# Performance work log

Hardware: AMD Instinct MI355X
Metric: run time of the kernel (lower is better)

The kernel has to match this reference:

```python
import jax, jax.numpy as jnp
import numpy as np

B, N, FI, F, NN, ITER = 128, 64, 8, 32, 64, 3
E = N * (N - 1)  # 4032 directed edges (fully connected, no self-loops)


def _p(k, shape):
    return jax.random.normal(k, shape, jnp.float32) / np.float32(np.sqrt(shape[0]))


def setup_inputs() -> dict:
    key = jax.random.key(0)
    ks = jax.random.split(key, 20)
    u_is = np.array([i for i in range(N) for j in range(N) if i != j], np.int32)
    u_js = np.array([j for i in range(N) for j in range(N) if i != j], np.int32)
    return {
        "node0": jax.random.normal(ks[0], (B, N, FI), jnp.float32),
        "edge": jax.random.normal(ks[1], (B, E, 2), jnp.float32),
        "node_mean": jax.random.normal(ks[2], (B, N, 1), jnp.float32),
        "node_vari": jax.random.uniform(ks[3], (B, N, 1), jnp.float32),
        "h": jax.random.normal(ks[4], (B, N, NN), jnp.float32),
        "W1": _p(ks[5], (FI, F)), "b1": jnp.zeros((F,), jnp.float32),
        "W2a": _p(ks[6], (2 * F + 2, NN)), "b2a": jnp.zeros((NN,), jnp.float32),
        "W2b": _p(ks[7], (NN, NN // 2)), "b2b": jnp.zeros((NN // 2,), jnp.float32),
        "W2c": _p(ks[8], (NN // 2, F)), "b2c": jnp.zeros((F,), jnp.float32),
        "Wx": _p(ks[9], (F, 3 * NN)), "Ux": _p(ks[10], (NN, 3 * NN)),
        "bx": jnp.zeros((3 * NN,), jnp.float32), "bh": jnp.zeros((3 * NN,), jnp.float32),
        "W3b": _p(ks[11], (NN, F)), "b3b": jnp.zeros((F,), jnp.float32),
        "W4a": _p(ks[12], (F, NN)), "b4a": jnp.zeros((NN,), jnp.float32),
        "W4b": _p(ks[13], (NN, NN // 2)), "b4b": jnp.zeros((NN // 2,), jnp.float32),
        "W4c": _p(ks[14], (NN // 2, F)), "b4c": jnp.zeros((F,), jnp.float32),
        "u_is": jnp.asarray(u_is), "u_js": jnp.asarray(u_js),
    }


def _forward(node0, edge, h, W1, b1, W2a, b2a, W2b, b2b, W2c, b2c,
             Wx, Ux, bx, bh, W3b, b3b, W4a, b4a, W4b, b4b, W4c, b4c,
             u_is, u_js):
    gelu = jax.nn.gelu
    node = node0 @ W1 + b1  # fc1a: [B,N,F]
    for _ in range(ITER):
        # gather source/target node features per directed edge, concat edge feats
        u_ij = jnp.concatenate([node[:, u_is, :], node[:, u_js, :], edge], -1)  # [B,E,2F+2]
        m = gelu(u_ij @ W2a + b2a)   # [B,E,NN]
        m = gelu(m @ W2b + b2b)      # [B,E,NN//2]
        m = gelu(m @ W2c + b2c)      # [B,E,F]
        # edges are ordered by source node i, so segment-sum == reshape+sum
        m_i = m.reshape(-1, N, N - 1, F).sum(-2)  # [B,N,F]
        # FlexGRU cell with GELU candidate activation (ACT_GELU)
        gx = m_i @ Wx + bx
        gh = h @ Ux + bh
        xr, xz, xn = jnp.split(gx, 3, -1)
        hr, hz, hn = jnp.split(gh, 3, -1)
        r = jax.nn.sigmoid(xr + hr)
        z = jax.nn.sigmoid(xz + hz)
        n = gelu(xn + r * hn)
        h = (1.0 - z) * n + z * h    # [B,N,NN]
        node = h @ W3b + b3b         # fc3b: [B,N,F]
    # readout: fc4a -> fc4b -> fc4c with no intermediate activation (as in source)
    return ((node @ W4a + b4a) @ W4b + b4b) @ W4c + b4c  # [B,N,F]


def reference(node0, edge, node_mean, node_vari, h, W1, b1, W2a, b2a, W2b, b2b,
              W2c, b2c, Wx, Ux, bx, bh, W3b, b3b, W4a, b4a, W4b, b4b, W4c, b4c,
              u_is, u_js):
    # node_mean / node_vari are accepted by the original forward but unused
    return _forward(node0, edge, h, W1, b1, W2a, b2a, W2b, b2b, W2c, b2c,
                    Wx, Ux, bx, bh, W3b, b3b, W4a, b4a, W4b, b4b, W4c, b4c,
                    u_is, u_js)
```

## Files before the change

kernel.cpp:

```cpp
#include <hip/hip_runtime.h>


typedef _Float16 f16;
typedef _Float16 h8 __attribute__((ext_vector_type(8)));
typedef float f4 __attribute__((ext_vector_type(4)));

#define MFMA16(a, b, c) __builtin_amdgcn_mfma_f32_16x16x32_f16(a, b, c, 0, 0, 0)
#define WFENCE()                        \
  do {                                  \
    __builtin_amdgcn_wave_barrier();    \
    __asm__ volatile("" ::: "memory");  \
  } while (0)

#define H_OFF 0
#define Q_OFF 2097152
#define P_OFF 4194304
#define WQ_OFF 6291456
#define O_W45B 0
#define O_W2BTH 768
#define O_W2BTL 4864
#define O_B2B 8960
#define O_W2CTH 9088
#define O_W2CTL 11136
#define O_B2C 13184

#define LI_M2W 0
#define LI_ND 0
#define LI_HN 1024
#define LI_T1 3072
#define LI_T2 5248
#define LI_W2BH 10240
#define LI_W2BL 14848
#define LI_W2CH 19456
#define LI_W2CL 22016
#define LI_MACC 24576
#define LI_H32 25600
#define LI_TOTAL 27648

__device__ __forceinline__ float fast_rcp(float x) {
#if __has_builtin(__builtin_amdgcn_rcpf)
  return __builtin_amdgcn_rcpf(x);
#else
  return 1.0f / x;
#endif
}
__device__ __forceinline__ float gelu_f(float x) {
  float x3 = x * x * x;
  float u = -1.5957691216057308f * fmaf(0.044715f, x3, x);
  return x * fast_rcp(1.f + __expf(u));
}
__device__ __forceinline__ float sigm_f(float x) {
  return fast_rcp(1.f + __expf(-x));
}
__device__ __forceinline__ void splitw(float v, f16& h, f16& l) {
  h = (f16)v;
  l = (f16)(v - (float)h);
}

__global__ __launch_bounds__(256) void k_pre(
    const float* __restrict__ node0, const float* __restrict__ W1,
    const float* __restrict__ b1, const float* __restrict__ W2a,
    const float* __restrict__ b2a, const float* __restrict__ W2b,
    const float* __restrict__ b2b, const float* __restrict__ W2c,
    const float* __restrict__ b2c, float* __restrict__ ws) {
  const int t = threadIdx.x;
  const int blk = blockIdx.x;
  char* wsb = (char*)ws;
  float* Qbuf = (float*)(wsb + Q_OFF);
  float* Pbuf = (float*)(wsb + P_OFF);
  char* W = wsb + WQ_OFF;

  if (blk < 256) {
    __shared__ float sNode[1024];
    const int b = blk >> 1;
    const int n0 = (blk & 1) << 5;
    for (int idx = t; idx < 1024; idx += 256) {
      const int n = idx >> 5, f = idx & 31;
      float acc = b1[f];
#pragma unroll
      for (int k = 0; k < 8; ++k)
        acc = fmaf(node0[((size_t)(b * 64 + n0 + n)) * 8 + k], W1[k * 32 + f], acc);
      sNode[idx] = acc;
    }
    __syncthreads();
    const int u = t & 63;
    const int sel = (t >> 6) & 1;
    const int nb = t >> 7;
    const float binit = sel ? 0.f : b2a[u];
    float acc[16];
#pragma unroll
    for (int o = 0; o < 16; ++o) acc[o] = binit;
    const float* wcol = W2a + (sel ? 2048 : 0) + u;
#pragma unroll 4
    for (int k = 0; k < 32; ++k) {
      const float w = wcol[k * 64];
#pragma unroll
      for (int o = 0; o < 16; ++o)
        acc[o] = fmaf(sNode[(nb + 2 * o) * 32 + k], w, acc[o]);
    }
    float* dst = sel ? Pbuf : Qbuf;
#pragma unroll
    for (int o = 0; o < 16; ++o)
      dst[((size_t)(b * 64 + n0 + nb + 2 * o)) * 64 + u] = acc[o];
  } else {
    float* wb = (float*)(W + O_W45B);
    if (t < 64) {
      wb[t] = W2a[64 * 64 + t];
      wb[64 + t] = W2a[65 * 64 + t];
      wb[128 + t] = b2a[t];
    }
    f16* bth = (f16*)(W + O_W2BTH);
    f16* btl = (f16*)(W + O_W2BTL);
    for (int idx = t; idx < 2048; idx += 256) {
      const int k = idx >> 5, v = idx & 31;
      f16 h_, l_;
      splitw(W2b[k * 32 + v], h_, l_);
      bth[v * 64 + k] = h_;
      btl[v * 64 + k] = l_;
    }
    float* b2bf = (float*)(W + O_B2B);
    if (t < 32) b2bf[t] = b2b[t];
    f16* cth = (f16*)(W + O_W2CTH);
    f16* ctl = (f16*)(W + O_W2CTL);
    for (int idx = t; idx < 1024; idx += 256) {
      const int k = idx >> 5, v = idx & 31;
      f16 h_, l_;
      splitw(W2c[k * 32 + v], h_, l_);
      cth[v * 32 + k] = h_;
      ctl[v * 32 + k] = l_;
    }
    float* b2cf = (float*)(W + O_B2C);
    if (t < 32) b2cf[t] = b2c[t];
  }
}

__global__ __launch_bounds__(256, 4) void k_iter(
    const float* __restrict__ edge, float* __restrict__ ws,
    const float* __restrict__ h_in, const float* __restrict__ Wx,
    const float* __restrict__ Ux, const float* __restrict__ bx,
    const float* __restrict__ bh, const float* __restrict__ W3b,
    const float* __restrict__ b3b, const float* __restrict__ W2a,
    const float* __restrict__ b2a, const float* __restrict__ W4a,
    const float* __restrict__ b4a, const float* __restrict__ W4b,
    const float* __restrict__ b4b, const float* __restrict__ W4c,
    const float* __restrict__ b4c, float* __restrict__ out, const int is_last) {
  __shared__ alignas(16) char sm[LI_TOTAL];
  f16* sW2BH = (f16*)(sm + LI_W2BH);
  f16* sW2BL = (f16*)(sm + LI_W2BL);
  f16* sW2CH = (f16*)(sm + LI_W2CH);
  f16* sW2CL = (f16*)(sm + LI_W2CL);
  float* sMacc = (float*)(sm + LI_MACC);
  float* sH32 = (float*)(sm + LI_H32);

  const int tid = threadIdx.x;
  const int lane = tid & 63;
  const int wave = tid >> 6;
  const int col = lane & 15;
  const int quad = lane >> 4;
  const int b = blockIdx.x >> 3;
  const int i0 = (blockIdx.x & 7) << 3;

  char* wsb = (char*)ws;
  float* h_ws = (float*)(wsb + H_OFF);
  float* Qbuf = (float*)(wsb + Q_OFF);
  float* Pbuf = (float*)(wsb + P_OFF);
  const char* W = wsb + WQ_OFF;
  const float* w45b = (const float*)(W + O_W45B);
  const f16* W2BTHg = (const f16*)(W + O_W2BTH);
  const f16* W2BTLg = (const f16*)(W + O_W2BTL);
  const float* b2b_g = (const float*)(W + O_B2B);
  const f16* W2CTHg = (const f16*)(W + O_W2CTH);
  const f16* W2CTLg = (const f16*)(W + O_W2CTL);
  const float* b2c_g = (const float*)(W + O_B2C);

  for (int idx = tid; idx < 1024; idx += 256) {
    const int v = idx >> 5, k2 = idx & 31;
    ((unsigned int*)sW2BH)[v * 36 + k2] = ((const unsigned int*)W2BTHg)[idx];
    ((unsigned int*)sW2BL)[v * 36 + k2] = ((const unsigned int*)W2BTLg)[idx];
  }
  for (int idx = tid; idx < 512; idx += 256) {
    const int v = idx >> 4, k2 = idx & 15;
    ((unsigned int*)sW2CH)[v * 20 + k2] = ((const unsigned int*)W2CTHg)[idx];
    ((unsigned int*)sW2CL)[v * 20 + k2] = ((const unsigned int*)W2CTLg)[idx];
  }
  if (tid < 128) {
    const int nl = tid >> 4;
    const int k4 = (tid & 15) * 4;
    *(float4*)(sH32 + tid * 4) =
        *(const float4*)(h_in + ((size_t)(b * 64 + i0 + nl)) * 64 + k4);
  }
  __syncthreads();

  const float bb2[2] = {b2b_g[col], b2b_g[16 + col]};
  const float bc2[2] = {b2c_g[col], b2c_g[16 + col]};
  f4 wav[2][2], wbv[2][2];
#pragma unroll
  for (int kh = 0; kh < 2; ++kh) {
#pragma unroll
    for (int p = 0; p < 2; ++p) {
      wav[kh][p] = *(const f4*)(w45b + kh * 32 + quad * 8 + p * 4);
      wbv[kh][p] = *(const f4*)(w45b + 64 + kh * 32 + quad * 8 + p * 4);
    }
  }
  f16* m2h = (f16*)(sm + LI_M2W + wave * 2560);
  f16* m2l = m2h + 640;

#pragma unroll 1
  for (int cc2 = 0; cc2 < 2; ++cc2) {
    const int c = wave + 4 * cc2;
    const int ig = i0 + c;
    f4 qb[2][2];
#pragma unroll
    for (int kh = 0; kh < 2; ++kh)
#pragma unroll
      for (int p = 0; p < 2; ++p)
        qb[kh][p] = *(const f4*)(Qbuf + ((size_t)(b * 64 + ig)) * 64 + kh * 32 +
                                 quad * 8 + p * 4);
    const float* erow = edge + ((size_t)b * 4032 + (size_t)ig * 63) * 2;
    float ev0[4], ev1[4];
#pragma unroll
    for (int mt = 0; mt < 4; ++mt) {
      const int ko = mt * 16 + col;
      if (ko < 63) {
        const float2 e = *(const float2*)(erow + ko * 2);
        ev0[mt] = e.x;
        ev1[mt] = e.y;
      } else {
        ev0[mt] = 0.f;
        ev1[mt] = 0.f;
      }
    }
    float racc[2] = {0.f, 0.f};
#pragma unroll
    for (int mt = 0; mt < 4; ++mt) {
      const int ko = mt * 16 + col;
      int j = ko + ((ko >= ig) ? 1 : 0);
      j = (j > 63) ? 63 : j;
      const float e0 = ev0[mt], e1 = ev1[mt];
      h8 ah[2], al[2];
#pragma unroll
      for (int kh = 0; kh < 2; ++kh) {
        const float* prow =
            Pbuf + ((size_t)(b * 64 + j)) * 64 + kh * 32 + quad * 8;
        const f4 p0 = *(const f4*)prow;
        const f4 p1 = *(const f4*)(prow + 4);
#pragma unroll
        for (int jj = 0; jj < 4; ++jj) {
          float v = qb[kh][0][jj] + p0[jj];
          v = fmaf(e1, wbv[kh][0][jj], fmaf(e0, wav[kh][0][jj], v));
          float g = gelu_f(v) * 0.015625f;
          f16 hi = (f16)g;
          ah[kh][jj] = hi;
          al[kh][jj] = (f16)(g - (float)hi);
          v = qb[kh][1][jj] + p1[jj];
          v = fmaf(e1, wbv[kh][1][jj], fmaf(e0, wav[kh][1][jj], v));
          g = gelu_f(v) * 0.015625f;
          hi = (f16)g;
          ah[kh][4 + jj] = hi;
          al[kh][4 + jj] = (f16)(g - (float)hi);
        }
      }
#pragma unroll
      for (int nt = 0; nt < 2; ++nt) {
        const f16* rbh = sW2BH + (nt * 16 + col) * 72 + quad * 8;
        const f16* rbl = sW2BL + (nt * 16 + col) * 72 + quad * 8;
        const h8 bh0 = *(const h8*)rbh;
        const h8 bh1 = *(const h8*)(rbh + 32);
        const h8 bl0 = *(const h8*)rbl;
        const h8 bl1 = *(const h8*)(rbl + 32);
        f4 cm = {0.f, 0.f, 0.f, 0.f};
        cm = MFMA16(ah[0], bh0, cm);
        cm = MFMA16(ah[1], bh1, cm);
        cm = MFMA16(ah[0], bl0, cm);
        cm = MFMA16(ah[1], bl1, cm);
        cm = MFMA16(al[0], bh0, cm);
        cm = MFMA16(al[1], bh1, cm);
#pragma unroll
        for (int r = 0; r < 4; ++r) {
          const float g = gelu_f(fmaf(64.f, cm[r], bb2[nt])) * 0.015625f;
          const f16 hi = (f16)g;
          const int o = (quad * 4 + r) * 40 + nt * 16 + col;
          m2h[o] = hi;
          m2l[o] = (f16)(g - (float)hi);
        }
      }
      WFENCE();
      const h8 a2h = *(const h8*)(m2h + col * 40 + quad * 8);
      const h8 a2l = *(const h8*)(m2l + col * 40 + quad * 8);
      WFENCE();
#pragma unroll
      for (int nt = 0; nt < 2; ++nt) {
        const h8 bch = *(const h8*)(sW2CH + (nt * 16 + col) * 40 + quad * 8);
        const h8 bcl = *(const h8*)(sW2CL + (nt * 16 + col) * 40 + quad * 8);
        f4 dm = {0.f, 0.f, 0.f, 0.f};
        dm = MFMA16(a2h, bch, dm);
        dm = MFMA16(a2h, bcl, dm);
        dm = MFMA16(a2l, bch, dm);
#pragma unroll
        for (int r = 0; r < 4; ++r) {
          const int slot3 = mt * 16 + quad * 4 + r;
          const float g = gelu_f(fmaf(64.f, dm[r], bc2[nt]));
          racc[nt] += (slot3 != 63) ? g : 0.f;
        }
      }
    }
    racc[0] += __shfl_xor(racc[0], 16);
    racc[0] += __shfl_xor(racc[0], 32);
    racc[1] += __shfl_xor(racc[1], 16);
    racc[1] += __shfl_xor(racc[1], 32);
    if (lane < 32) sMacc[c * 32 + lane] = (lane < 16) ? racc[0] : racc[1];
  }
  __syncthreads();

  float* sHn = (float*)(sm + LI_HN);
  {
    const int u = lane;
    const float bxr = bx[u], bhr = bh[u];
    const float bxz = bx[64 + u], bhz = bh[64 + u];
    const float bxn = bx[128 + u], bhn = bh[128 + u];
#pragma unroll 1
    for (int p = 0; p < 2; ++p) {
      const int n0 = wave + 4 * p;
      float axr = 0.f, axz = 0.f, axn = 0.f;
#pragma unroll 4
      for (int k = 0; k < 32; ++k) {
        const float m0 = sMacc[n0 * 32 + k];
        axr = fmaf(m0, Wx[k * 192 + u], axr);
        axz = fmaf(m0, Wx[k * 192 + 64 + u], axz);
        axn = fmaf(m0, Wx[k * 192 + 128 + u], axn);
      }
      float ahr = 0.f, ahz = 0.f, ahn = 0.f;
#pragma unroll 4
      for (int k = 0; k < 64; ++k) {
        const float h0 = sH32[n0 * 64 + k];
        ahr = fmaf(h0, Ux[k * 192 + u], ahr);
        ahz = fmaf(h0, Ux[k * 192 + 64 + u], ahz);
        ahn = fmaf(h0, Ux[k * 192 + 128 + u], ahn);
      }
      const float r_ = sigm_f(axr + ahr + bxr + bhr);
      const float z_ = sigm_f(axz + ahz + bxz + bhz);
      const float n_ = gelu_f(fmaf(r_, ahn + bhn, axn + bxn));
      const float hold = sH32[n0 * 64 + u];
      const float hnew = (1.f - z_) * n_ + z_ * hold;
      sHn[n0 * 64 + u] = hnew;
      if (!is_last) h_ws[((size_t)(b * 64 + i0 + n0)) * 64 + u] = hnew;
    }
  }
  __syncthreads();

  float* sNd = (float*)(sm + LI_ND);
  {
    const int nn = tid >> 5, f = tid & 31;
    float acc = b3b[f];
#pragma unroll 8
    for (int k = 0; k < 64; ++k)
      acc = fmaf(sHn[nn * 64 + k], W3b[k * 32 + f], acc);
    sNd[nn * 32 + f] = acc;
  }
  __syncthreads();

  if (!is_last) {
    const int u = lane;
    const int sel = (tid >> 6) & 1;
    const int nb = tid >> 7;
    const float binit = sel ? 0.f : b2a[u];
    float acc[4] = {binit, binit, binit, binit};
    const float* wcol = W2a + (sel ? 2048 : 0) + u;
#pragma unroll 4
    for (int k = 0; k < 32; ++k) {
      const float w = wcol[k * 64];
      acc[0] = fmaf(sNd[(nb + 0) * 32 + k], w, acc[0]);
      acc[1] = fmaf(sNd[(nb + 2) * 32 + k], w, acc[1]);
      acc[2] = fmaf(sNd[(nb + 4) * 32 + k], w, acc[2]);
      acc[3] = fmaf(sNd[(nb + 6) * 32 + k], w, acc[3]);
    }
    float* dst = sel ? Pbuf : Qbuf;
#pragma unroll
    for (int o = 0; o < 4; ++o)
      dst[((size_t)(b * 64 + i0 + nb + 2 * o)) * 64 + u] = acc[o];
  } else {
    float* sT1 = (float*)(sm + LI_T1);
    float* sT2 = (float*)(sm + LI_T2);
    {
      const int u = lane;
      float acc0 = b4a[u], acc1 = b4a[u];
#pragma unroll 4
      for (int k = 0; k < 32; ++k) {
        const float w = W4a[k * 64 + u];
        acc0 = fmaf(sNd[wave * 32 + k], w, acc0);
        acc1 = fmaf(sNd[(wave + 4) * 32 + k], w, acc1);
      }
      sT1[wave * 68 + u] = acc0;
      sT1[(wave + 4) * 68 + u] = acc1;
    }
    __syncthreads();
    {
      const int nn = tid >> 5, v = tid & 31;
      float acc = b4b[v];
#pragma unroll 8
      for (int k = 0; k < 64; ++k)
        acc = fmaf(sT1[nn * 68 + k], W4b[k * 32 + v], acc);
      sT2[nn * 36 + v] = acc;
    }
    __syncthreads();
    {
      const int nn = tid >> 5, f = tid & 31;
      float acc = b4c[f];
#pragma unroll 8
      for (int k = 0; k < 32; ++k)
        acc = fmaf(sT2[nn * 36 + k], W4c[k * 32 + f], acc);
      out[((size_t)(b * 64 + i0 + nn)) * 32 + f] = acc;
    }
  }
}

extern "C" void kernel_launch(void* const* d_in, const int* in_sizes, int n_in,
                              void* d_out, int out_size, void* d_ws, size_t ws_size,
                              hipStream_t stream) {
  (void)in_sizes;
  (void)n_in;
  (void)out_size;
  (void)ws_size;
  const float* node0 = (const float*)d_in[0];
  const float* edge = (const float*)d_in[1];
  const float* hin = (const float*)d_in[4];
  const float* W1 = (const float*)d_in[5];
  const float* b1 = (const float*)d_in[6];
  const float* W2a = (const float*)d_in[7];
  const float* b2a = (const float*)d_in[8];
  const float* W2b = (const float*)d_in[9];
  const float* b2b = (const float*)d_in[10];
  const float* W2c = (const float*)d_in[11];
  const float* b2c = (const float*)d_in[12];
  const float* Wx = (const float*)d_in[13];
  const float* Ux = (const float*)d_in[14];
  const float* bx = (const float*)d_in[15];
  const float* bh = (const float*)d_in[16];
  const float* W3b = (const float*)d_in[17];
  const float* b3b = (const float*)d_in[18];
  const float* W4a = (const float*)d_in[19];
  const float* b4a = (const float*)d_in[20];
  const float* W4b = (const float*)d_in[21];
  const float* b4b = (const float*)d_in[22];
  const float* W4c = (const float*)d_in[23];
  const float* b4c = (const float*)d_in[24];

  float* ws = (float*)d_ws;
  char* wsb = (char*)d_ws;
  float* h_ws = (float*)(wsb + H_OFF);
  float* out = (float*)d_out;

  k_pre<<<dim3(257), dim3(256), 0, stream>>>(node0, W1, b1, W2a, b2a, W2b, b2b, W2c,
                                             b2c, ws);
  k_iter<<<dim3(1024), dim3(256), 0, stream>>>(edge, ws, hin, Wx, Ux, bx, bh, W3b,
                                               b3b, W2a, b2a, W4a, b4a, W4b, b4b,
                                               W4c, b4c, nullptr, 0);
  k_iter<<<dim3(1024), dim3(256), 0, stream>>>(edge, ws, h_ws, Wx, Ux, bx, bh, W3b,
                                               b3b, W2a, b2a, W4a, b4a, W4b, b4b,
                                               W4c, b4c, nullptr, 0);
  k_iter<<<dim3(1024), dim3(256), 0, stream>>>(edge, ws, h_ws, Wx, Ux, bx, bh, W3b,
                                               b3b, W2a, b2a, W4a, b4a, W4b, b4b,
                                               W4c, b4c, out, 1);
}
```

Baseline: 281.1 us.

## Keep W2c fragments in registers, shrink LDS, raise occupancy, split k_pre finer

```diff
diff --git a/kernel.cpp b/kernel.cpp
--- a/kernel.cpp
+++ b/kernel.cpp
@@ -31,11 +31,9 @@
 #define LI_T2 5248
 #define LI_W2BH 10240
 #define LI_W2BL 14848
-#define LI_W2CH 19456
-#define LI_W2CL 22016
-#define LI_MACC 24576
-#define LI_H32 25600
-#define LI_TOTAL 27648
+#define LI_MACC 19456
+#define LI_H32 20480
+#define LI_TOTAL 22528
 
 __device__ __forceinline__ float fast_rcp(float x) {
 #if __has_builtin(__builtin_amdgcn_rcpf)
@@ -70,37 +68,36 @@
   float* Pbuf = (float*)(wsb + P_OFF);
   char* W = wsb + WQ_OFF;
 
-  if (blk < 256) {
-    __shared__ float sNode[1024];
-    const int b = blk >> 1;
-    const int n0 = (blk & 1) << 5;
-    for (int idx = t; idx < 1024; idx += 256) {
-      const int n = idx >> 5, f = idx & 31;
+  if (blk < 1024) {
+    __shared__ float sNode[256];
+    const int b = blk >> 3;
+    const int n0 = (blk & 7) << 3;
+    {
+      const int n = t >> 5, f = t & 31;
       float acc = b1[f];
 #pragma unroll
       for (int k = 0; k < 8; ++k)
         acc = fmaf(node0[((size_t)(b * 64 + n0 + n)) * 8 + k], W1[k * 32 + f], acc);
-      sNode[idx] = acc;
+      sNode[n * 32 + f] = acc;
     }
     __syncthreads();
     const int u = t & 63;
     const int sel = (t >> 6) & 1;
     const int nb = t >> 7;
     const float binit = sel ? 0.f : b2a[u];
-    float acc[16];
-#pragma unroll
-    for (int o = 0; o < 16; ++o) acc[o] = binit;
+    float acc[4] = {binit, binit, binit, binit};
     const float* wcol = W2a + (sel ? 2048 : 0) + u;
 #pragma unroll 4
     for (int k = 0; k < 32; ++k) {
       const float w = wcol[k * 64];
-#pragma unroll
-      for (int o = 0; o < 16; ++o)
-        acc[o] = fmaf(sNode[(nb + 2 * o) * 32 + k], w, acc[o]);
+      acc[0] = fmaf(sNode[(nb + 0) * 32 + k], w, acc[0]);
+      acc[1] = fmaf(sNode[(nb + 2) * 32 + k], w, acc[1]);
+      acc[2] = fmaf(sNode[(nb + 4) * 32 + k], w, acc[2]);
+      acc[3] = fmaf(sNode[(nb + 6) * 32 + k], w, acc[3]);
     }
     float* dst = sel ? Pbuf : Qbuf;
 #pragma unroll
-    for (int o = 0; o < 16; ++o)
+    for (int o = 0; o < 4; ++o)
       dst[((size_t)(b * 64 + n0 + nb + 2 * o)) * 64 + u] = acc[o];
   } else {
     float* wb = (float*)(W + O_W45B);
@@ -134,7 +131,7 @@
   }
 }
 
-__global__ __launch_bounds__(256, 4) void k_iter(
+__global__ __launch_bounds__(256, 5) void k_iter(
     const float* __restrict__ edge, float* __restrict__ ws,
     const float* __restrict__ h_in, const float* __restrict__ Wx,
     const float* __restrict__ Ux, const float* __restrict__ bx,
@@ -147,8 +144,6 @@
   __shared__ alignas(16) char sm[LI_TOTAL];
   f16* sW2BH = (f16*)(sm + LI_W2BH);
   f16* sW2BL = (f16*)(sm + LI_W2BL);
-  f16* sW2CH = (f16*)(sm + LI_W2CH);
-  f16* sW2CL = (f16*)(sm + LI_W2CL);
   float* sMacc = (float*)(sm + LI_MACC);
   float* sH32 = (float*)(sm + LI_H32);
 
@@ -178,11 +173,6 @@
     ((unsigned int*)sW2BH)[v * 36 + k2] = ((const unsigned int*)W2BTHg)[idx];
     ((unsigned int*)sW2BL)[v * 36 + k2] = ((const unsigned int*)W2BTLg)[idx];
   }
-  for (int idx = tid; idx < 512; idx += 256) {
-    const int v = idx >> 4, k2 = idx & 15;
-    ((unsigned int*)sW2CH)[v * 20 + k2] = ((const unsigned int*)W2CTHg)[idx];
-    ((unsigned int*)sW2CL)[v * 20 + k2] = ((const unsigned int*)W2CTLg)[idx];
-  }
   if (tid < 128) {
     const int nl = tid >> 4;
     const int k4 = (tid & 15) * 4;
@@ -193,6 +183,12 @@
 
   const float bb2[2] = {b2b_g[col], b2b_g[16 + col]};
   const float bc2[2] = {b2c_g[col], b2c_g[16 + col]};
+  h8 Bch[2], Bcl[2];
+#pragma unroll
+  for (int nt = 0; nt < 2; ++nt) {
+    Bch[nt] = *(const h8*)(W2CTHg + (nt * 16 + col) * 32 + quad * 8);
+    Bcl[nt] = *(const h8*)(W2CTLg + (nt * 16 + col) * 32 + quad * 8);
+  }
   f4 wav[2][2], wbv[2][2];
 #pragma unroll
   for (int kh = 0; kh < 2; ++kh) {
@@ -290,12 +286,10 @@
       WFENCE();
 #pragma unroll
       for (int nt = 0; nt < 2; ++nt) {
-        const h8 bch = *(const h8*)(sW2CH + (nt * 16 + col) * 40 + quad * 8);
-        const h8 bcl = *(const h8*)(sW2CL + (nt * 16 + col) * 40 + quad * 8);
         f4 dm = {0.f, 0.f, 0.f, 0.f};
-        dm = MFMA16(a2h, bch, dm);
-        dm = MFMA16(a2h, bcl, dm);
-        dm = MFMA16(a2l, bch, dm);
+        dm = MFMA16(a2h, Bch[nt], dm);
+        dm = MFMA16(a2h, Bcl[nt], dm);
+        dm = MFMA16(a2l, Bch[nt], dm);
 #pragma unroll
         for (int r = 0; r < 4; ++r) {
           const int slot3 = mt * 16 + quad * 4 + r;
@@ -450,8 +444,8 @@
   float* h_ws = (float*)(wsb + H_OFF);
   float* out = (float*)d_out;
 
-  k_pre<<<dim3(257), dim3(256), 0, stream>>>(node0, W1, b1, W2a, b2a, W2b, b2b, W2c,
-                                             b2c, ws);
+  k_pre<<<dim3(1025), dim3(256), 0, stream>>>(node0, W1, b1, W2a, b2a, W2b, b2b,
+                                              W2c, b2c, ws);
   k_iter<<<dim3(1024), dim3(256), 0, stream>>>(edge, ws, hin, Wx, Ux, bx, bh, W3b,
                                                b3b, W2a, b2a, W4a, b4a, W4b, b4b,
                                                W4c, b4c, nullptr, 0);
```

After: 428.2 us. 1.52x slower.
